# Kernel optimization log

Measured on AMD Instinct MI355X. Metric: run time of the kernel, lower is better.

Reference implementation:

```python
import jax, jax.numpy as jnp
import numpy as np

B, L, D, H, LAYERS = 4, 1024, 512, 8, 6
HD = D // H           # 64
E = H * HD            # 512 (hid_dim)
F = 4 * D             # 2048 (ffn hidden)
EPS = 1e-5


def _layernorm(x, g, b):
    m = jnp.mean(x, axis=-1, keepdims=True)
    v = jnp.mean((x - m) ** 2, axis=-1, keepdims=True)
    return (x - m) * jax.lax.rsqrt(v + EPS) * g + b


def setup_inputs() -> dict:
    key0 = jax.random.key(0)
    ks = jax.random.split(key0, 20)
    query = jax.random.normal(ks[0], (B, L, D), dtype=jnp.float32)
    key_t = jax.random.normal(ks[1], (B, L, D), dtype=jnp.float32)
    # ragged valid lengths so masking paths are exercised
    lengths = jnp.array([1024, 896, 768, 640], dtype=jnp.int32)
    pos = jnp.arange(L)[None, :]
    query_mask = (pos < lengths[:, None]).astype(jnp.float32)
    key_mask = query_mask
    s = 0.02
    p = {
        'Wq': jax.random.normal(ks[2], (LAYERS, E, D)) * s,
        'bq': jax.random.normal(ks[3], (LAYERS, E)) * s,
        'Wk': jax.random.normal(ks[4], (LAYERS, E, D)) * s,
        'bk': jax.random.normal(ks[5], (LAYERS, E)) * s,
        'Wv': jax.random.normal(ks[6], (LAYERS, E, D)) * s,
        'bv': jax.random.normal(ks[7], (LAYERS, E)) * s,
        'Wo': jax.random.normal(ks[8], (LAYERS, D, E)) * s,
        'bo': jax.random.normal(ks[9], (LAYERS, D)) * s,
        'W1': jax.random.normal(ks[10], (LAYERS, F, D)) * s,
        'b1': jax.random.normal(ks[11], (LAYERS, F)) * s,
        'W2': jax.random.normal(ks[12], (LAYERS, D, F)) * s,
        'b2': jax.random.normal(ks[13], (LAYERS, D)) * s,
        'ln1_g': jnp.ones((LAYERS, D), jnp.float32),
        'ln1_b': jnp.zeros((LAYERS, D), jnp.float32),
        'ln2_g': jnp.ones((LAYERS, D), jnp.float32),
        'ln2_b': jnp.zeros((LAYERS, D), jnp.float32),
    }
    p = {k: v.astype(jnp.float32) for k, v in p.items()}
    return {'query': query, 'key': key_t, 'query_mask': query_mask, 'key_mask': key_mask, **p}


def reference(query, key, query_mask, key_mask,
              Wq, bq, Wk, bk, Wv, bv, Wo, bo,
              W1, b1, W2, b2, ln1_g, ln1_b, ln2_g, ln2_b):
    b, lq, d = query.shape
    scale = jnp.float32(HD) ** -0.5
    kmask0 = (key_mask == 0)[:, None, None, :]  # [B,1,1,Tk]
    qm = query_mask[:, :, None]                  # [B,Tq,1]
    x = query
    for i in range(LAYERS):
        # qkv projections (Conv1d kernel_size=1 == per-token linear)
        q = (jnp.einsum('bld,ed->ble', x, Wq[i]) + bq[i]).reshape(b, lq, H, HD).transpose(0, 2, 1, 3)
        k = (jnp.einsum('bld,ed->ble', key, Wk[i]) + bk[i]).reshape(b, -1, H, HD).transpose(0, 2, 1, 3)
        v = (jnp.einsum('bld,ed->ble', key, Wv[i]) + bv[i]).reshape(b, -1, H, HD).transpose(0, 2, 1, 3)
        scores = jnp.einsum('bhqd,bhkd->bhqk', q * scale, k)  # [B,H,Tq,Tk]
        scores = jnp.where(kmask0, -jnp.inf, scores)
        attn = jax.nn.softmax(scores, axis=-1)
        out = jnp.einsum('bhqk,bhkd->bhqd', attn, v)
        out = out.transpose(0, 2, 1, 3).reshape(b, lq, E)
        out = jnp.einsum('ble,de->bld', out, Wo[i]) + bo[i]
        out = out * qm
        x = _layernorm(out + x, ln1_g[i], ln1_b[i])
        # FFN
        h = jax.nn.relu(jnp.einsum('bld,fd->blf', x, W1[i]) + b1[i])
        f = jnp.einsum('blf,df->bld', h, W2[i]) + b2[i]
        f = f * qm
        x = _layernorm(f + x, ln2_g[i], ln2_b[i])
    return x
```

## Files before the change

kernel.cpp:

```cpp
#include <hip/hip_runtime.h>
#include <stdint.h>

typedef unsigned short u16;
typedef __bf16 bf16_t;
typedef bf16_t v8bf __attribute__((ext_vector_type(8)));
typedef u16    v8u  __attribute__((ext_vector_type(8)));
typedef float  v4f  __attribute__((ext_vector_type(4)));

#define NLAYERS 6
#define LN_EPS 1e-5f
#define NROWS 4096
#define ND 512
#define NF 2048
#define QKV_LD 1536

static constexpr size_t WQKV = 0;
static constexpr size_t WOo  = 4718592;
static constexpr size_t W1o  = 6291456;
static constexpr size_t W2o  = 12582912;
static constexpr size_t BQKV = 18874368;
static constexpr size_t BOo  = BQKV + 9216;
static constexpr size_t B1o  = BOo + 3072;
static constexpr size_t B2o  = B1o + 12288;
static constexpr size_t L1G  = B2o + 3072, L1B = L1G + 3072;
static constexpr size_t L2G  = L1B + 3072, L2B = L2G + 3072;
static constexpr size_t QMo  = L2B + 3072;

__device__ __forceinline__ float b2f(u16 u){
  union { unsigned int i; float f; } x; x.i = ((unsigned int)u) << 16; return x.f;
}
__device__ __forceinline__ u16 f2b(float f){
  union { float f; unsigned int i; } x; x.f = f;
  unsigned int u = x.i;
  return (u16)((u + 0x7fffu + ((u >> 16) & 1u)) >> 16);
}

__device__ __forceinline__ void gl_lds16(const u16* g, u16* l){
  __builtin_amdgcn_global_load_lds(
      (const __attribute__((address_space(1))) unsigned int*)(g),
      (__attribute__((address_space(3))) unsigned int*)(l), 16, 0, 0);
}

__global__ __launch_bounds__(256) void conv_lin(
    const float* __restrict__ src, u16* __restrict__ dst, int n)
{
  const int i = (blockIdx.x * 256 + threadIdx.x) * 8;
  if (i >= n) return;
  float4 x0 = *(const float4*)(src + i);
  float4 x1 = *(const float4*)(src + i + 4);
  v8u o;
  o[0]=f2b(x0.x); o[1]=f2b(x0.y); o[2]=f2b(x0.z); o[3]=f2b(x0.w);
  o[4]=f2b(x1.x); o[5]=f2b(x1.y); o[6]=f2b(x1.z); o[7]=f2b(x1.w);
  *(v8u*)(dst + i) = o;
}

__global__ __launch_bounds__(256) void conv_strided(
    const float* __restrict__ src, u16* __restrict__ dst,
    int n, int lshift, int dstStride, int dstOff)
{
  const int i = (blockIdx.x * 256 + threadIdx.x) * 8;
  if (i >= n) return;
  const int layer  = i >> lshift;
  const int within = i & ((1 << lshift) - 1);
  u16* d = dst + (size_t)layer * dstStride + dstOff + within;
  float4 x0 = *(const float4*)(src + i);
  float4 x1 = *(const float4*)(src + i + 4);
  v8u o;
  o[0]=f2b(x0.x); o[1]=f2b(x0.y); o[2]=f2b(x0.z); o[3]=f2b(x0.w);
  o[4]=f2b(x1.x); o[5]=f2b(x1.y); o[6]=f2b(x1.z); o[7]=f2b(x1.w);
  *(v8u*)d = o;
}

__global__ __launch_bounds__(256) void conv_small(
    const float* __restrict__ bqs, const float* __restrict__ bks,
    const float* __restrict__ bvs, const float* __restrict__ bos,
    const float* __restrict__ b1s, const float* __restrict__ b2s,
    const float* __restrict__ g1,  const float* __restrict__ be1,
    const float* __restrict__ g2,  const float* __restrict__ be2,
    u16* __restrict__ wcan)
{
  const int v = blockIdx.x * 256 + threadIdx.x;
  if (v >= 4992) return;
  const int i = v * 8;
  const float* src; size_t dst;
  if (i < 9216){
    const int part = i / 3072;
    const int j = i - part * 3072;
    src = (part == 0 ? bqs : part == 1 ? bks : bvs) + j;
    dst = BQKV + (size_t)(j >> 9) * 1536 + part * 512 + (j & 511);
  } else if (i < 12288){ const int j = i -  9216; src = bos + j; dst = BOo + j; }
  else if (i < 24576){ const int j = i - 12288; src = b1s + j; dst = B1o + j; }
  else if (i < 27648){ const int j = i - 24576; src = b2s + j; dst = B2o + j; }
  else if (i < 30720){ const int j = i - 27648; src = g1  + j; dst = L1G + j; }
  else if (i < 33792){ const int j = i - 30720; src = be1 + j; dst = L1B + j; }
  else if (i < 36864){ const int j = i - 33792; src = g2  + j; dst = L2G + j; }
  else               { const int j = i - 36864; src = be2 + j; dst = L2B + j; }
  float4 x0 = *(const float4*)(src);
  float4 x1 = *(const float4*)(src + 4);
  v8u o;
  o[0]=f2b(x0.x); o[1]=f2b(x0.y); o[2]=f2b(x0.z); o[3]=f2b(x0.w);
  o[4]=f2b(x1.x); o[5]=f2b(x1.y); o[6]=f2b(x1.z); o[7]=f2b(x1.w);
  *(v8u*)(wcan + dst) = o;
}

__global__ void compute_len(const float* __restrict__ qm, int* __restrict__ len){
  __shared__ int cnt;
  if (threadIdx.x == 0) cnt = 0;
  __syncthreads();
  int c = 0;
  const int b = blockIdx.x;
  for (int i = threadIdx.x; i < 1024; i += 256)
    if (qm[b * 1024 + i] != 0.f) c++;
  atomicAdd(&cnt, c);
  __syncthreads();
  if (threadIdx.x == 0) len[b] = cnt;
}

__global__ __launch_bounds__(256) void copy_out_f32(
    const u16* __restrict__ x, float* __restrict__ out)
{
  const int i = (blockIdx.x * 256 + threadIdx.x) * 8;
  v8u v = *(const v8u*)(x + i);
  float4 a, b;
  a.x=b2f(v[0]); a.y=b2f(v[1]); a.z=b2f(v[2]); a.w=b2f(v[3]);
  b.x=b2f(v[4]); b.y=b2f(v[5]); b.z=b2f(v[6]); b.w=b2f(v[7]);
  *(float4*)(out + i) = a;
  *(float4*)(out + i + 4) = b;
}

template<int MT, int NT, int RELU, int QKV>
__global__ __launch_bounds__(256) void gemm_k(
    const u16* __restrict__ A0, const u16* __restrict__ A1,
    const u16* __restrict__ W, const u16* __restrict__ bias,
    u16* __restrict__ C, u16* __restrict__ VT,
    const int* __restrict__ len_g, int ldc, int K)
{
  constexpr int WM = MT / 2, WN = NT / 2;
  constexpr int NI = WM / 16, NJ = WN / 16;
  constexpr int RA = MT / 64, RB = NT / 64;
  __shared__ __align__(16) u16 As[MT * 32];
  __shared__ __align__(16) u16 Bs[NT * 32];

  const int t    = threadIdx.x;
  const int lane = t & 63, wave = t >> 6;
  const int ln   = lane & 15, quad = lane >> 4;
  const int n0 = blockIdx.x * NT;
  const int m0 = blockIdx.y * MT;
  if ((m0 & 1023) >= len_g[m0 >> 10]) return;

  const u16* A = (QKV && n0 >= 512) ? A1 : A0;
  const int wm = wave & 1, wn = wave >> 1;

  v4f acc[NI][NJ];
  #pragma unroll
  for (int i = 0; i < NI; ++i)
    #pragma unroll
    for (int j = 0; j < NJ; ++j) acc[i][j] = (v4f){0.f,0.f,0.f,0.f};

  const u16* aS[RA]; const u16* bS[RB];
  #pragma unroll
  for (int ra = 0; ra < RA; ++ra){
    const int u = t + ra * 256;
    aS[ra] = A + (size_t)(m0 + (u >> 2)) * K + (u & 3) * 8;
  }
  #pragma unroll
  for (int rb = 0; rb < RB; ++rb){
    const int u = t + rb * 256;
    bS[rb] = W + (size_t)(n0 + (u >> 2)) * K + (u & 3) * 8;
  }

  for (int k0 = 0; k0 < K; k0 += 32){
    #pragma unroll
    for (int ra = 0; ra < RA; ++ra) gl_lds16(aS[ra] + k0, &As[(t + ra*256) * 8]);
    #pragma unroll
    for (int rb = 0; rb < RB; ++rb) gl_lds16(bS[rb] + k0, &Bs[(t + rb*256) * 8]);
    __syncthreads();

    v8bf a[NI], bf[NJ];
    #pragma unroll
    for (int i = 0; i < NI; ++i)
      a[i] = *(const v8bf*)&As[(wm * WM + i * 16 + ln) * 32 + quad * 8];
    #pragma unroll
    for (int j = 0; j < NJ; ++j)
      bf[j] = *(const v8bf*)&Bs[(wn * WN + j * 16 + ln) * 32 + quad * 8];
    #pragma unroll
    for (int i = 0; i < NI; ++i)
      #pragma unroll
      for (int j = 0; j < NJ; ++j)
        acc[i][j] = __builtin_amdgcn_mfma_f32_16x16x32_bf16(a[i], bf[j], acc[i][j], 0, 0, 0);
    __syncthreads();
  }

  #pragma unroll
  for (int j = 0; j < NJ; ++j){
    const int col = n0 + wn * WN + j * 16 + ln;
    const float bs = b2f(bias[col]);
    #pragma unroll
    for (int i = 0; i < NI; ++i){
      #pragma unroll
      for (int r = 0; r < 4; ++r){
        const int row = m0 + wm * WM + i * 16 + quad * 4 + r;
        float v = acc[i][j][r] + bs;
        if (RELU) v = fmaxf(v, 0.f);
        if (QKV && col >= 1024){
          const int e = col - 1024;
          VT[(((size_t)(row >> 10) * 8 + (e >> 6)) * 64 + (e & 63)) * 1024 + (row & 1023)] = f2b(v);
        } else {
          C[(size_t)row * ldc + col] = f2b(v);
        }
      }
    }
  }
}

__global__ __launch_bounds__(256) void attn_kernel(
    const u16* __restrict__ qkv, const u16* __restrict__ VT,
    const int* __restrict__ len_g, u16* __restrict__ O)
{
  __shared__ __align__(16) u16 Ks[64 * 72];
  __shared__ __align__(16) u16 Vs[64 * 72];
  __shared__ __align__(16) u16 Pl[4][16 * 72];

  const int t    = threadIdx.x;
  const int lane = t & 63, wave = t >> 6;
  const int ln   = lane & 15, quad = lane >> 4;
  const int bh = blockIdx.x >> 4;
  const int qc = blockIdx.x & 15;
  const int h = bh & 7, b = bh >> 3;
  const int len = len_g[b];
  if (qc * 64 >= len) return;
  const int q0 = qc * 64 + wave * 16;

  const u16* Qb = qkv + ((size_t)b * 1024 + q0 + ln) * QKV_LD + h * 64;
  const v8bf aq0 = *(const v8bf*)(Qb + quad * 8);
  const v8bf aq1 = *(const v8bf*)(Qb + 32 + quad * 8);

  const u16* Kbase = qkv + (size_t)b * 1024 * QKV_LD + 512 + h * 64;
  const u16* Vbase = VT + (size_t)bh * 64 * 1024;

  const int r0 = t >> 3,         c0 = (t & 7) * 8;
  const int r1 = (t + 256) >> 3, c1 = c0;
  const u16* Kst0 = Kbase + (size_t)r0 * QKV_LD + c0;
  const u16* Kst1 = Kbase + (size_t)r1 * QKV_LD + c1;
  const u16* Vst0 = Vbase + (size_t)r0 * 1024 + c0;
  const u16* Vst1 = Vbase + (size_t)r1 * 1024 + c1;
  u16* KsD0 = &Ks[r0 * 72 + c0]; u16* KsD1 = &Ks[r1 * 72 + c1];
  u16* VsD0 = &Vs[r0 * 72 + c0]; u16* VsD1 = &Vs[r1 * 72 + c1];

  float m_i[4], l_i[4];
  #pragma unroll
  for (int r = 0; r < 4; ++r){ m_i[r] = -1e30f; l_i[r] = 0.f; }
  v4f o_acc[4];
  #pragma unroll
  for (int c = 0; c < 4; ++c) o_acc[c] = (v4f){0.f,0.f,0.f,0.f};

  u16* P = Pl[wave];

  v8u ck0 = *(const v8u*)Kst0;
  v8u ck1 = *(const v8u*)Kst1;
  v8u cv0 = *(const v8u*)Vst0;
  v8u cv1 = *(const v8u*)Vst1;

  for (int j0 = 0; j0 < len; j0 += 64){
    __syncthreads();
    *(v8u*)KsD0 = ck0; *(v8u*)KsD1 = ck1;
    *(v8u*)VsD0 = cv0; *(v8u*)VsD1 = cv1;
    __syncthreads();

    const int jn = j0 + 64;
    if (jn < len){
      ck0 = *(const v8u*)(Kst0 + (size_t)jn * QKV_LD);
      ck1 = *(const v8u*)(Kst1 + (size_t)jn * QKV_LD);
      cv0 = *(const v8u*)(Vst0 + jn);
      cv1 = *(const v8u*)(Vst1 + jn);
    }

    const bool tail = (len - j0) < 64;

    v4f s[4];
    #pragma unroll
    for (int st = 0; st < 4; ++st){
      const u16* kr = &Ks[(st * 16 + ln) * 72];
      v4f ss = {0.f,0.f,0.f,0.f};
      ss = __builtin_amdgcn_mfma_f32_16x16x32_bf16(aq0, *(const v8bf*)(kr + quad * 8),      ss, 0,0,0);
      ss = __builtin_amdgcn_mfma_f32_16x16x32_bf16(aq1, *(const v8bf*)(kr + 32 + quad * 8), ss, 0,0,0);
      s[st] = ss;
    }

    float p[4][4], mt[4];
    #pragma unroll
    for (int r = 0; r < 4; ++r) mt[r] = -1e30f;
    #pragma unroll
    for (int st = 0; st < 4; ++st){
      const bool dead = tail && (j0 + st * 16 + ln) >= len;
      #pragma unroll
      for (int r = 0; r < 4; ++r){
        float sc = dead ? -1e30f : s[st][r] * 0.125f;
        p[st][r] = sc;
        mt[r] = fmaxf(mt[r], sc);
      }
    }
    #pragma unroll
    for (int off = 1; off < 16; off <<= 1)
      #pragma unroll
      for (int r = 0; r < 4; ++r) mt[r] = fmaxf(mt[r], __shfl_xor(mt[r], off));

    float alpha[4], ts[4];
    #pragma unroll
    for (int r = 0; r < 4; ++r){
      const float mn = fmaxf(m_i[r], mt[r]);
      alpha[r] = __expf(m_i[r] - mn);
      m_i[r] = mn;
    }
    #pragma unroll
    for (int st = 0; st < 4; ++st)
      #pragma unroll
      for (int r = 0; r < 4; ++r) p[st][r] = __expf(p[st][r] - m_i[r]);
    #pragma unroll
    for (int r = 0; r < 4; ++r) ts[r] = (p[0][r] + p[1][r]) + (p[2][r] + p[3][r]);
    #pragma unroll
    for (int off = 1; off < 16; off <<= 1)
      #pragma unroll
      for (int r = 0; r < 4; ++r) ts[r] += __shfl_xor(ts[r], off);
    #pragma unroll
    for (int r = 0; r < 4; ++r) l_i[r] = l_i[r] * alpha[r] + ts[r];
    #pragma unroll
    for (int c = 0; c < 4; ++c)
      #pragma unroll
      for (int r = 0; r < 4; ++r) o_acc[c][r] *= alpha[r];

    #pragma unroll
    for (int st = 0; st < 4; ++st)
      #pragma unroll
      for (int r = 0; r < 4; ++r)
        P[(quad * 4 + r) * 72 + st * 16 + ln] = f2b(p[st][r]);
    const v8bf ap0 = *(const v8bf*)&P[ln * 72 + quad * 8];
    const v8bf ap1 = *(const v8bf*)&P[ln * 72 + 32 + quad * 8];

    #pragma unroll
    for (int c = 0; c < 4; ++c){
      const u16* vr = &Vs[(c * 16 + ln) * 72];
      o_acc[c] = __builtin_amdgcn_mfma_f32_16x16x32_bf16(ap0, *(const v8bf*)(vr + quad * 8),      o_acc[c], 0,0,0);
      o_acc[c] = __builtin_amdgcn_mfma_f32_16x16x32_bf16(ap1, *(const v8bf*)(vr + 32 + quad * 8), o_acc[c], 0,0,0);
    }
  }

  u16* Ob = O + ((size_t)b * 1024 + q0) * 512 + h * 64;
  #pragma unroll
  for (int c = 0; c < 4; ++c)
    #pragma unroll
    for (int r = 0; r < 4; ++r)
      Ob[(size_t)(quad * 4 + r) * 512 + c * 16 + ln] = f2b(o_acc[c][r] / l_i[r]);
}

__global__ __launch_bounds__(256) void ln_res(
    const u16* __restrict__ Y, const u16* __restrict__ qm,
    const u16* __restrict__ g, const u16* __restrict__ beta,
    u16* __restrict__ X)
{
  const int lane = threadIdx.x & 63;
  const int wave = threadIdx.x >> 6;
  const int row  = blockIdx.x * 4 + wave;

  const float qv = b2f(qm[row]);
  const u16* y = Y + (size_t)row * ND;
  u16*       x = X + (size_t)row * ND;

  v8u yv = *(const v8u*)(y + lane * 8);
  v8u xv = *(const v8u*)(x + lane * 8);
  float tt[8]; float s = 0.f, s2 = 0.f;
  #pragma unroll
  for (int i = 0; i < 8; ++i){
    tt[i] = b2f(yv[i]) * qv + b2f(xv[i]);
    s  += tt[i];
    s2 += tt[i] * tt[i];
  }
  #pragma unroll
  for (int off = 1; off < 64; off <<= 1){
    s  += __shfl_xor(s,  off);
    s2 += __shfl_xor(s2, off);
  }
  const float mean = s * (1.f / ND);
  const float var  = fmaxf(s2 * (1.f / ND) - mean * mean, 0.f);
  const float inv  = rsqrtf(var + LN_EPS);

  v8u gv = *(const v8u*)(g    + lane * 8);
  v8u bv = *(const v8u*)(beta + lane * 8);
  v8u ov;
  #pragma unroll
  for (int i = 0; i < 8; ++i)
    ov[i] = f2b((tt[i] - mean) * inv * b2f(gv[i]) + b2f(bv[i]));
  *(v8u*)(x + lane * 8) = ov;
}

extern "C" void kernel_launch(void* const* d_in, const int* in_sizes, int n_in,
                              void* d_out, int out_size, void* d_ws, size_t ws_size,
                              hipStream_t stream)
{
  char* ws = (char*)d_ws;
  const size_t MiB = 1u << 20;
  u16* qkv = (u16*)(ws);
  u16* VT  = (u16*)(ws + 12 * MiB);
  u16* hb  = (u16*)(ws);
  u16* tb1 = (u16*)(ws);
  u16* xb   = (u16*)(ws + 16 * MiB);
  u16* kcan = (u16*)(ws + 20 * MiB);
  u16* ob   = (u16*)(ws + 24 * MiB);
  u16* tb2  = ob;
  u16* wcan = (u16*)(ws + 28 * MiB);
  int* len  = (int*)(ws + 65 * MiB);

  const float* f_query = (const float*)d_in[0];
  const float* f_key   = (const float*)d_in[1];
  const float* f_qm    = (const float*)d_in[2];

  conv_lin<<<1024, 256, 0, stream>>>(f_query, xb,   NROWS * ND);
  conv_lin<<<1024, 256, 0, stream>>>(f_key,   kcan, NROWS * ND);
  conv_lin<<<2,    256, 0, stream>>>(f_qm, wcan + QMo, NROWS);

  conv_strided<<<768, 256, 0, stream>>>((const float*)d_in[4], wcan + WQKV, 1572864, 18, 786432, 0);
  conv_strided<<<768, 256, 0, stream>>>((const float*)d_in[6], wcan + WQKV, 1572864, 18, 786432, 262144);
  conv_strided<<<768, 256, 0, stream>>>((const float*)d_in[8], wcan + WQKV, 1572864, 18, 786432, 524288);

  conv_lin<<<768,  256, 0, stream>>>((const float*)d_in[10], wcan + WOo, 1572864);
  conv_lin<<<3072, 256, 0, stream>>>((const float*)d_in[12], wcan + W1o, 6291456);
  conv_lin<<<3072, 256, 0, stream>>>((const float*)d_in[14], wcan + W2o, 6291456);

  conv_small<<<20, 256, 0, stream>>>(
      (const float*)d_in[5],  (const float*)d_in[7],  (const float*)d_in[9],
      (const float*)d_in[11], (const float*)d_in[13], (const float*)d_in[15],
      (const float*)d_in[16], (const float*)d_in[17],
      (const float*)d_in[18], (const float*)d_in[19], wcan);

  compute_len<<<4, 256, 0, stream>>>(f_qm, len);

  for (int i = 0; i < NLAYERS; ++i){
    const u16* Wqkv_i = wcan + WQKV + (size_t)i * 786432;
    const u16* bqkv_i = wcan + BQKV + (size_t)i * 1536;
    const u16* Wo_i = wcan + WOo + (size_t)i * 262144;
    const u16* W1_i = wcan + W1o + (size_t)i * 1048576;
    const u16* W2_i = wcan + W2o + (size_t)i * 1048576;

    gemm_k<64,128,0,1><<<dim3(12, 64), 256, 0, stream>>>(
        xb, kcan, Wqkv_i, bqkv_i, qkv, VT, len, QKV_LD, ND);

    attn_kernel<<<512, 256, 0, stream>>>(qkv, VT, len, ob);

    gemm_k<64,64,0,0><<<dim3(8, 64), 256, 0, stream>>>(
        ob, ob, Wo_i, wcan + BOo + (size_t)i * ND, tb1, nullptr, len, ND, ND);
    ln_res<<<NROWS / 4, 256, 0, stream>>>(tb1, wcan + QMo,
        wcan + L1G + (size_t)i * ND, wcan + L1B + (size_t)i * ND, xb);

    gemm_k<128,128,1,0><<<dim3(16, 32), 256, 0, stream>>>(
        xb, xb, W1_i, wcan + B1o + (size_t)i * NF, hb, nullptr, len, NF, ND);
    gemm_k<64,64,0,0><<<dim3(8, 64), 256, 0, stream>>>(
        hb, hb, W2_i, wcan + B2o + (size_t)i * ND, tb2, nullptr, len, ND, NF);
    ln_res<<<NROWS / 4, 256, 0, stream>>>(tb2, wcan + QMo,
        wcan + L2G + (size_t)i * ND, wcan + L2B + (size_t)i * ND, xb);
  }

  copy_out_f32<<<1024, 256, 0, stream>>>(xb, (float*)d_out);
}
```

Measured before the change: 840.1 us.

## Use 128x128 GEMM tiles everywhere, merge conversion kernels, fuse final output cast

All GEMMs now use one 128x128 tile configuration, including the QKV, Wo and W2 projections, so each block reuses more of its loaded data but fewer blocks are launched for the N=512 GEMMs. The separate weight and input conversion kernels are merged into three larger launches, and the mask conversion moves into conv_small, to cut launch overhead. The final layernorm writes fp32 output directly, which removes the copy_out kernel and keeps the last layer's result unrounded. The risk is lower occupancy on the narrow GEMMs, for example only 128 blocks for Wo and W2.

```diff
diff --git a/kernel.cpp b/kernel.cpp
--- a/kernel.cpp
+++ b/kernel.cpp
@@ -41,34 +41,45 @@
       (__attribute__((address_space(3))) unsigned int*)(l), 16, 0, 0);
 }
 
-__global__ __launch_bounds__(256) void conv_lin(
-    const float* __restrict__ src, u16* __restrict__ dst, int n)
-{
-  const int i = (blockIdx.x * 256 + threadIdx.x) * 8;
-  if (i >= n) return;
-  float4 x0 = *(const float4*)(src + i);
-  float4 x1 = *(const float4*)(src + i + 4);
+__device__ __forceinline__ void cvt8(const float* __restrict__ src, u16* __restrict__ dst){
+  float4 x0 = *(const float4*)(src);
+  float4 x1 = *(const float4*)(src + 4);
   v8u o;
   o[0]=f2b(x0.x); o[1]=f2b(x0.y); o[2]=f2b(x0.z); o[3]=f2b(x0.w);
   o[4]=f2b(x1.x); o[5]=f2b(x1.y); o[6]=f2b(x1.z); o[7]=f2b(x1.w);
-  *(v8u*)(dst + i) = o;
-}
-
-__global__ __launch_bounds__(256) void conv_strided(
-    const float* __restrict__ src, u16* __restrict__ dst,
-    int n, int lshift, int dstStride, int dstOff)
+  *(v8u*)dst = o;
+}
+
+__global__ __launch_bounds__(256) void conv_qk(
+    const float* __restrict__ q, const float* __restrict__ k,
+    u16* __restrict__ xb, u16* __restrict__ kcan)
 {
   const int i = (blockIdx.x * 256 + threadIdx.x) * 8;
-  if (i >= n) return;
-  const int layer  = i >> lshift;
-  const int within = i & ((1 << lshift) - 1);
-  u16* d = dst + (size_t)layer * dstStride + dstOff + within;
-  float4 x0 = *(const float4*)(src + i);
-  float4 x1 = *(const float4*)(src + i + 4);
-  v8u o;
-  o[0]=f2b(x0.x); o[1]=f2b(x0.y); o[2]=f2b(x0.z); o[3]=f2b(x0.w);
-  o[4]=f2b(x1.x); o[5]=f2b(x1.y); o[6]=f2b(x1.z); o[7]=f2b(x1.w);
-  *(v8u*)d = o;
+  if (i < 2097152) cvt8(q + i, xb + i);
+  else             cvt8(k + (i - 2097152), kcan + (i - 2097152));
+}
+
+__global__ __launch_bounds__(256) void conv_qkvw(
+    const float* __restrict__ wq, const float* __restrict__ wk,
+    const float* __restrict__ wv, u16* __restrict__ wcan)
+{
+  const int i = (blockIdx.x * 256 + threadIdx.x) * 8;
+  const float* src; int part, j;
+  if (i < 1572864){ part = 0; j = i;           src = wq + j; }
+  else if (i < 3145728){ part = 1; j = i - 1572864; src = wk + j; }
+  else { part = 2; j = i - 3145728; src = wv + j; }
+  const int layer = j >> 18, within = j & 262143;
+  cvt8(src, wcan + WQKV + (size_t)layer * 786432 + part * 262144 + within);
+}
+
+__global__ __launch_bounds__(256) void conv_w3(
+    const float* __restrict__ wo, const float* __restrict__ w1,
+    const float* __restrict__ w2, u16* __restrict__ wcan)
+{
+  const int i = (blockIdx.x * 256 + threadIdx.x) * 8;
+  if (i < 1572864)      cvt8(wo + i, wcan + WOo + i);
+  else if (i < 7864320) cvt8(w1 + (i - 1572864), wcan + W1o + (i - 1572864));
+  else                  cvt8(w2 + (i - 7864320), wcan + W2o + (i - 7864320));
 }
 
 __global__ __launch_bounds__(256) void conv_small(
@@ -77,10 +88,10 @@
     const float* __restrict__ b1s, const float* __restrict__ b2s,
     const float* __restrict__ g1,  const float* __restrict__ be1,
     const float* __restrict__ g2,  const float* __restrict__ be2,
-    u16* __restrict__ wcan)
+    const float* __restrict__ qm,  u16* __restrict__ wcan)
 {
   const int v = blockIdx.x * 256 + threadIdx.x;
-  if (v >= 4992) return;
+  if (v >= 5504) return;
   const int i = v * 8;
   const float* src; size_t dst;
   if (i < 9216){
@@ -94,13 +105,9 @@
   else if (i < 30720){ const int j = i - 27648; src = g1  + j; dst = L1G + j; }
   else if (i < 33792){ const int j = i - 30720; src = be1 + j; dst = L1B + j; }
   else if (i < 36864){ const int j = i - 33792; src = g2  + j; dst = L2G + j; }
-  else               { const int j = i - 36864; src = be2 + j; dst = L2B + j; }
-  float4 x0 = *(const float4*)(src);
-  float4 x1 = *(const float4*)(src + 4);
-  v8u o;
-  o[0]=f2b(x0.x); o[1]=f2b(x0.y); o[2]=f2b(x0.z); o[3]=f2b(x0.w);
-  o[4]=f2b(x1.x); o[5]=f2b(x1.y); o[6]=f2b(x1.z); o[7]=f2b(x1.w);
-  *(v8u*)(wcan + dst) = o;
+  else if (i < 39936){ const int j = i - 36864; src = be2 + j; dst = L2B + j; }
+  else               { const int j = i - 39936; src = qm  + j; dst = QMo + j; }
+  cvt8(src, wcan + dst);
 }
 
 __global__ void compute_len(const float* __restrict__ qm, int* __restrict__ len){
@@ -116,90 +123,69 @@
   if (threadIdx.x == 0) len[b] = cnt;
 }
 
-__global__ __launch_bounds__(256) void copy_out_f32(
-    const u16* __restrict__ x, float* __restrict__ out)
-{
-  const int i = (blockIdx.x * 256 + threadIdx.x) * 8;
-  v8u v = *(const v8u*)(x + i);
-  float4 a, b;
-  a.x=b2f(v[0]); a.y=b2f(v[1]); a.z=b2f(v[2]); a.w=b2f(v[3]);
-  b.x=b2f(v[4]); b.y=b2f(v[5]); b.z=b2f(v[6]); b.w=b2f(v[7]);
-  *(float4*)(out + i) = a;
-  *(float4*)(out + i + 4) = b;
-}
-
-template<int MT, int NT, int RELU, int QKV>
+template<int RELU, int QKV>
 __global__ __launch_bounds__(256) void gemm_k(
     const u16* __restrict__ A0, const u16* __restrict__ A1,
     const u16* __restrict__ W, const u16* __restrict__ bias,
     u16* __restrict__ C, u16* __restrict__ VT,
     const int* __restrict__ len_g, int ldc, int K)
 {
-  constexpr int WM = MT / 2, WN = NT / 2;
-  constexpr int NI = WM / 16, NJ = WN / 16;
-  constexpr int RA = MT / 64, RB = NT / 64;
-  __shared__ __align__(16) u16 As[MT * 32];
-  __shared__ __align__(16) u16 Bs[NT * 32];
+  __shared__ __align__(16) u16 As[128 * 32];
+  __shared__ __align__(16) u16 Bs[128 * 32];
 
   const int t    = threadIdx.x;
   const int lane = t & 63, wave = t >> 6;
   const int ln   = lane & 15, quad = lane >> 4;
-  const int n0 = blockIdx.x * NT;
-  const int m0 = blockIdx.y * MT;
+  const int n0 = blockIdx.x * 128;
+  const int m0 = blockIdx.y * 128;
   if ((m0 & 1023) >= len_g[m0 >> 10]) return;
 
   const u16* A = (QKV && n0 >= 512) ? A1 : A0;
   const int wm = wave & 1, wn = wave >> 1;
 
-  v4f acc[NI][NJ];
-  #pragma unroll
-  for (int i = 0; i < NI; ++i)
-    #pragma unroll
-    for (int j = 0; j < NJ; ++j) acc[i][j] = (v4f){0.f,0.f,0.f,0.f};
-
-  const u16* aS[RA]; const u16* bS[RB];
-  #pragma unroll
-  for (int ra = 0; ra < RA; ++ra){
-    const int u = t + ra * 256;
-    aS[ra] = A + (size_t)(m0 + (u >> 2)) * K + (u & 3) * 8;
-  }
-  #pragma unroll
-  for (int rb = 0; rb < RB; ++rb){
-    const int u = t + rb * 256;
-    bS[rb] = W + (size_t)(n0 + (u >> 2)) * K + (u & 3) * 8;
-  }
+  v4f acc[4][4];
+  #pragma unroll
+  for (int i = 0; i < 4; ++i)
+    #pragma unroll
+    for (int j = 0; j < 4; ++j) acc[i][j] = (v4f){0.f,0.f,0.f,0.f};
+
+  const int u0 = t, u1 = t + 256;
+  const u16* aS0 = A + (size_t)(m0 + (u0 >> 2)) * K + (u0 & 3) * 8;
+  const u16* aS1 = A + (size_t)(m0 + (u1 >> 2)) * K + (u1 & 3) * 8;
+  const u16* bS0 = W + (size_t)(n0 + (u0 >> 2)) * K + (u0 & 3) * 8;
+  const u16* bS1 = W + (size_t)(n0 + (u1 >> 2)) * K + (u1 & 3) * 8;
 
   for (int k0 = 0; k0 < K; k0 += 32){
-    #pragma unroll
-    for (int ra = 0; ra < RA; ++ra) gl_lds16(aS[ra] + k0, &As[(t + ra*256) * 8]);
-    #pragma unroll
-    for (int rb = 0; rb < RB; ++rb) gl_lds16(bS[rb] + k0, &Bs[(t + rb*256) * 8]);
+    gl_lds16(aS0 + k0, &As[u0 * 8]);
+    gl_lds16(aS1 + k0, &As[u1 * 8]);
+    gl_lds16(bS0 + k0, &Bs[u0 * 8]);
+    gl_lds16(bS1 + k0, &Bs[u1 * 8]);
     __syncthreads();
 
-    v8bf a[NI], bf[NJ];
-    #pragma unroll
-    for (int i = 0; i < NI; ++i)
-      a[i] = *(const v8bf*)&As[(wm * WM + i * 16 + ln) * 32 + quad * 8];
-    #pragma unroll
-    for (int j = 0; j < NJ; ++j)
-      bf[j] = *(const v8bf*)&Bs[(wn * WN + j * 16 + ln) * 32 + quad * 8];
-    #pragma unroll
-    for (int i = 0; i < NI; ++i)
-      #pragma unroll
-      for (int j = 0; j < NJ; ++j)
+    v8bf a[4], bf[4];
+    #pragma unroll
+    for (int i = 0; i < 4; ++i)
+      a[i] = *(const v8bf*)&As[(wm * 64 + i * 16 + ln) * 32 + quad * 8];
+    #pragma unroll
+    for (int j = 0; j < 4; ++j)
+      bf[j] = *(const v8bf*)&Bs[(wn * 64 + j * 16 + ln) * 32 + quad * 8];
+    #pragma unroll
+    for (int i = 0; i < 4; ++i)
+      #pragma unroll
+      for (int j = 0; j < 4; ++j)
         acc[i][j] = __builtin_amdgcn_mfma_f32_16x16x32_bf16(a[i], bf[j], acc[i][j], 0, 0, 0);
     __syncthreads();
   }
 
   #pragma unroll
-  for (int j = 0; j < NJ; ++j){
-    const int col = n0 + wn * WN + j * 16 + ln;
+  for (int j = 0; j < 4; ++j){
+    const int col = n0 + wn * 64 + j * 16 + ln;
     const float bs = b2f(bias[col]);
     #pragma unroll
-    for (int i = 0; i < NI; ++i){
+    for (int i = 0; i < 4; ++i){
       #pragma unroll
       for (int r = 0; r < 4; ++r){
-        const int row = m0 + wm * WM + i * 16 + quad * 4 + r;
+        const int row = m0 + wm * 64 + i * 16 + quad * 4 + r;
         float v = acc[i][j][r] + bs;
         if (RELU) v = fmaxf(v, 0.f);
         if (QKV && col >= 1024){
@@ -353,10 +339,11 @@
       Ob[(size_t)(quad * 4 + r) * 512 + c * 16 + ln] = f2b(o_acc[c][r] / l_i[r]);
 }
 
+template<int OUT>
 __global__ __launch_bounds__(256) void ln_res(
     const u16* __restrict__ Y, const u16* __restrict__ qm,
     const u16* __restrict__ g, const u16* __restrict__ beta,
-    u16* __restrict__ X)
+    u16* __restrict__ X, float* __restrict__ fout)
 {
   const int lane = threadIdx.x & 63;
   const int wave = threadIdx.x >> 6;
@@ -386,11 +373,24 @@
 
   v8u gv = *(const v8u*)(g    + lane * 8);
   v8u bv = *(const v8u*)(beta + lane * 8);
-  v8u ov;
+  float ov[8];
   #pragma unroll
   for (int i = 0; i < 8; ++i)
-    ov[i] = f2b((tt[i] - mean) * inv * b2f(gv[i]) + b2f(bv[i]));
-  *(v8u*)(x + lane * 8) = ov;
+    ov[i] = (tt[i] - mean) * inv * b2f(gv[i]) + b2f(bv[i]);
+
+  if (OUT){
+    float4 o0, o1;
+    o0.x=ov[0]; o0.y=ov[1]; o0.z=ov[2]; o0.w=ov[3];
+    o1.x=ov[4]; o1.y=ov[5]; o1.z=ov[6]; o1.w=ov[7];
+    float* fo = fout + (size_t)row * ND + lane * 8;
+    *(float4*)fo = o0;
+    *(float4*)(fo + 4) = o1;
+  } else {
+    v8u o;
+    #pragma unroll
+    for (int i = 0; i < 8; ++i) o[i] = f2b(ov[i]);
+    *(v8u*)(x + lane * 8) = o;
+  }
 }
 
 extern "C" void kernel_launch(void* const* d_in, const int* in_sizes, int n_in,
@@ -410,28 +410,18 @@
   u16* wcan = (u16*)(ws + 28 * MiB);
   int* len  = (int*)(ws + 65 * MiB);
 
-  const float* f_query = (const float*)d_in[0];
-  const float* f_key   = (const float*)d_in[1];
-  const float* f_qm    = (const float*)d_in[2];
-
-  conv_lin<<<1024, 256, 0, stream>>>(f_query, xb,   NROWS * ND);
-  conv_lin<<<1024, 256, 0, stream>>>(f_key,   kcan, NROWS * ND);
-  conv_lin<<<2,    256, 0, stream>>>(f_qm, wcan + QMo, NROWS);
-
-  conv_strided<<<768, 256, 0, stream>>>((const float*)d_in[4], wcan + WQKV, 1572864, 18, 786432, 0);
-  conv_strided<<<768, 256, 0, stream>>>((const float*)d_in[6], wcan + WQKV, 1572864, 18, 786432, 262144);
-  conv_strided<<<768, 256, 0, stream>>>((const float*)d_in[8], wcan + WQKV, 1572864, 18, 786432, 524288);
-
-  conv_lin<<<768,  256, 0, stream>>>((const float*)d_in[10], wcan + WOo, 1572864);
-  conv_lin<<<3072, 256, 0, stream>>>((const float*)d_in[12], wcan + W1o, 6291456);
-  conv_lin<<<3072, 256, 0, stream>>>((const float*)d_in[14], wcan + W2o, 6291456);
-
-  conv_small<<<20, 256, 0, stream>>>(
+  const float* f_qm = (const float*)d_in[2];
+
+  conv_qk<<<2048, 256, 0, stream>>>((const float*)d_in[0], (const float*)d_in[1], xb, kcan);
+  conv_qkvw<<<2304, 256, 0, stream>>>((const float*)d_in[4], (const float*)d_in[6],
+                                      (const float*)d_in[8], wcan);
+  conv_w3<<<6912, 256, 0, stream>>>((const float*)d_in[10], (const float*)d_in[12],
+                                    (const float*)d_in[14], wcan);
+  conv_small<<<22, 256, 0, stream>>>(
       (const float*)d_in[5],  (const float*)d_in[7],  (const float*)d_in[9],
       (const float*)d_in[11], (const float*)d_in[13], (const float*)d_in[15],
       (const float*)d_in[16], (const float*)d_in[17],
-      (const float*)d_in[18], (const float*)d_in[19], wcan);
-
+      (const float*)d_in[18], (const float*)d_in[19], f_qm, wcan);
   compute_len<<<4, 256, 0, stream>>>(f_qm, len);
 
   for (int i = 0; i < NLAYERS; ++i){
@@ -441,23 +431,26 @@
     const u16* W1_i = wcan + W1o + (size_t)i * 1048576;
     const u16* W2_i = wcan + W2o + (size_t)i * 1048576;
 
-    gemm_k<64,128,0,1><<<dim3(12, 64), 256, 0, stream>>>(
+    gemm_k<0,1><<<dim3(12, 32), 256, 0, stream>>>(
         xb, kcan, Wqkv_i, bqkv_i, qkv, VT, len, QKV_LD, ND);
 
     attn_kernel<<<512, 256, 0, stream>>>(qkv, VT, len, ob);
 
-    gemm_k<64,64,0,0><<<dim3(8, 64), 256, 0, stream>>>(
+    gemm_k<0,0><<<dim3(4, 32), 256, 0, stream>>>(
         ob, ob, Wo_i, wcan + BOo + (size_t)i * ND, tb1, nullptr, len, ND, ND);
-    ln_res<<<NROWS / 4, 256, 0, stream>>>(tb1, wcan + QMo,
-        wcan + L1G + (size_t)i * ND, wcan + L1B + (size_t)i * ND, xb);
-
-    gemm_k<128,128,1,0><<<dim3(16, 32), 256, 0, stream>>>(
+    ln_res<0><<<NROWS / 4, 256, 0, stream>>>(tb1, wcan + QMo,
+        wcan + L1G + (size_t)i * ND, wcan + L1B + (size_t)i * ND, xb, nullptr);
+
+    gemm_k<1,0><<<dim3(16, 32), 256, 0, stream>>>(
         xb, xb, W1_i, wcan + B1o + (size_t)i * NF, hb, nullptr, len, NF, ND);
-    gemm_k<64,64,0,0><<<dim3(8, 64), 256, 0, stream>>>(
+    gemm_k<0,0><<<dim3(4, 32), 256, 0, stream>>>(
         hb, hb, W2_i, wcan + B2o + (size_t)i * ND, tb2, nullptr, len, ND, NF);
-    ln_res<<<NROWS / 4, 256, 0, stream>>>(tb2, wcan + QMo,
-        wcan + L2G + (size_t)i * ND, wcan + L2B + (size_t)i * ND, xb);
-  }
-
-  copy_out_f32<<<1024, 256, 0, stream>>>(xb, (float*)d_out);
-}
+
+    if (i < NLAYERS - 1)
+      ln_res<0><<<NROWS / 4, 256, 0, stream>>>(tb2, wcan + QMo,
+          wcan + L2G + (size_t)i * ND, wcan + L2B + (size_t)i * ND, xb, nullptr);
+    else
+      ln_res<1><<<NROWS / 4, 256, 0, stream>>>(tb2, wcan + QMo,
+          wcan + L2G + (size_t)i * ND, wcan + L2B + (size_t)i * ND, xb, (float*)d_out);
+  }
+}
```

New measurement: 991.1 us. 1.18x slower.
